# Kernel optimization log

Hardware: AMD Instinct MI355X
Metric: run time of the kernel (lower is better)

The kernel has to match this reference:

```python
import jax, jax.numpy as jnp
import numpy as np
import math

GROUPS = 32
EPS = 1e-5
N_HEADS = 8  # channels=512 / num_head_channels=64


def group_norm(x, w, b):
    # x: [B, C, T]; GroupNorm over (channels-in-group, T)
    B, C, T = x.shape
    xg = x.reshape(B, GROUPS, C // GROUPS * T)
    mu = xg.mean(axis=-1, keepdims=True)
    var = xg.var(axis=-1, keepdims=True)
    xn = ((xg - mu) * jax.lax.rsqrt(var + EPS)).reshape(B, C, T)
    return xn * w[None, :, None] + b[None, :, None]


def setup_inputs() -> dict:
    key = jax.random.key(0)
    ks = jax.random.split(key, 7)
    C = 512
    return {
        "x": jax.random.normal(ks[0], (8, C, 32, 32), dtype=jnp.float32),
        "norm_w": jax.random.normal(ks[1], (C,), dtype=jnp.float32),
        "norm_b": jax.random.normal(ks[2], (C,), dtype=jnp.float32),
        "qkv_w": jax.random.normal(ks[3], (3 * C, C), dtype=jnp.float32) * 0.02,
        "qkv_b": jax.random.normal(ks[4], (3 * C,), dtype=jnp.float32) * 0.02,
        "proj_w": jax.random.normal(ks[5], (C, C), dtype=jnp.float32) * 0.02,
        "proj_b": jax.random.normal(ks[6], (C,), dtype=jnp.float32) * 0.02,
    }


def reference(x, norm_w, norm_b, qkv_w, qkv_b, proj_w, proj_b):
    b, c, H, W = x.shape
    T = H * W
    xf = x.reshape(b, c, T)
    xn = group_norm(xf, norm_w, norm_b)
    # 1x1 conv1d == channel matmul: [3C, C] x [B, C, T] -> [B, 3C, T]
    qkv = jnp.einsum('oc,bct->bot', qkv_w, xn) + qkv_b[None, :, None]
    ch = c // N_HEADS
    qkv = qkv.reshape(b * N_HEADS, 3 * ch, T)
    q, k, v = qkv[:, :ch], qkv[:, ch:2 * ch], qkv[:, 2 * ch:]
    scale = 1.0 / math.sqrt(math.sqrt(ch))
    # [BH, T, T] score matrix (explicit, as in the original)
    weight = jnp.einsum('bct,bcs->bts', q * scale, k * scale)
    weight = jax.nn.softmax(weight.astype(jnp.float32), axis=-1).astype(qkv.dtype)
    a = jnp.einsum('bts,bcs->bct', weight, v).reshape(b, c, T)
    hout = jnp.einsum('oc,bct->bot', proj_w, a) + proj_b[None, :, None]
    return (xf + hout).reshape(b, c, H, W)
```

## Files before the change

### kernel.cpp

```cpp
#include <hip/hip_runtime.h>
#include <math.h>

typedef float f32x4_t __attribute__((ext_vector_type(4)));
typedef short bf16x8_t __attribute__((ext_vector_type(8)));

#define B_   8
#define C_   512
#define T_   1024
#define NH_  8
#define CH_  64
#define EPSF 1e-5f

#define MFMA16(a, b, c) __builtin_amdgcn_mfma_f32_16x16x32_bf16((a), (b), (c), 0, 0, 0)

__device__ __forceinline__ unsigned short f2bf(float f) {
  union { float f; unsigned u; } v; v.f = f;
  unsigned r = v.u + 0x7FFFu + ((v.u >> 16) & 1u);
  return (unsigned short)(r >> 16);
}

typedef const unsigned int u32_g __attribute__((address_space(1)));
typedef unsigned int u32_l __attribute__((address_space(3)));
__device__ __forceinline__ void gld16(const unsigned short* g, unsigned short* l) {
  __builtin_amdgcn_global_load_lds((u32_g*)g, (u32_l*)l, 16, 0, 0);
}
__device__ __forceinline__ void load_tile(const unsigned short* g,
                                          unsigned short* l, int tid) {
  int wb = (tid >> 6) * 512;
  gld16(g + tid * 8,        l + wb);
  gld16(g + 2048 + tid * 8, l + 2048 + wb);
}

__global__ __launch_bounds__(256) void prep_gn_kernel(
    const float* __restrict__ x, const float* __restrict__ w,
    const float* __restrict__ bvec, unsigned short* __restrict__ xnP,
    const float* __restrict__ qw_f, const float* __restrict__ pw_f,
    unsigned short* __restrict__ qwP, unsigned short* __restrict__ pwP)
{
  int tid = threadIdx.x;
  if (blockIdx.x >= 256) {
    int idx = (blockIdx.x - 256) * 256 + tid;
    const int N1 = 1536 * 512 / 4;
    const int N2 = 512 * 512 / 4;
    if (idx < N1) {
      float4 v = ((const float4*)qw_f)[idx];
      int o = idx >> 7, cq = (idx & 127) * 4;
      uint2 ov;
      ov.x = (unsigned)f2bf(v.x) | ((unsigned)f2bf(v.y) << 16);
      ov.y = (unsigned)f2bf(v.z) | ((unsigned)f2bf(v.w) << 16);
      *(uint2*)&qwP[((size_t)(cq >> 5) * 1536 + o) * 32 + (cq & 31)] = ov;
    } else if (idx < N1 + N2) {
      int j = idx - N1;
      float4 v = ((const float4*)pw_f)[j];
      int o = j >> 7, cq = (j & 127) * 4;
      uint2 ov;
      ov.x = (unsigned)f2bf(v.x) | ((unsigned)f2bf(v.y) << 16);
      ov.y = (unsigned)f2bf(v.z) | ((unsigned)f2bf(v.w) << 16);
      *(uint2*)&pwP[((size_t)(cq >> 5) * 512 + o) * 32 + (cq & 31)] = ov;
    }
    return;
  }

  int blk = blockIdx.x;
  int b = blk >> 5, g = blk & 31;
  const float* xp = x + ((size_t)(b * C_ + g * 16)) * T_;
  const int N = 16 * T_;

  float s = 0.f, s2 = 0.f;
  for (int i = tid * 4; i < N; i += 256 * 4) {
    float4 v = *(const float4*)(xp + i);
    s  += v.x + v.y + v.z + v.w;
    s2 += v.x * v.x + v.y * v.y + v.z * v.z + v.w * v.w;
  }
  for (int off = 32; off; off >>= 1) {
    s  += __shfl_down(s,  off, 64);
    s2 += __shfl_down(s2, off, 64);
  }
  __shared__ float rs_[4], r2_[4];
  __shared__ float mu_s, rsig_s;
  int wid = tid >> 6, lane = tid & 63;
  if (lane == 0) { rs_[wid] = s; r2_[wid] = s2; }
  __syncthreads();
  if (tid == 0) {
    float ts = rs_[0] + rs_[1] + rs_[2] + rs_[3];
    float t2 = r2_[0] + r2_[1] + r2_[2] + r2_[3];
    float mu = ts / (float)N;
    float var = t2 / (float)N - mu * mu;
    mu_s = mu;
    rsig_s = rsqrtf(var + EPSF);
  }
  __syncthreads();
  float mu = mu_s, rs = rsig_s;

  float wl[16], bl[16];
  for (int c = 0; c < 16; ++c) { wl[c] = w[g * 16 + c]; bl[c] = bvec[g * 16 + c]; }

  unsigned short* dbase = xnP + ((size_t)(b * 16 + (g >> 1)) * T_) * 32 + (g & 1) * 16;
  for (int t = tid; t < T_; t += 256) {
    unsigned short buf[16] __attribute__((aligned(16)));
    for (int c = 0; c < 16; ++c) {
      float val = xp[(size_t)c * T_ + t];
      buf[c] = f2bf((val - mu) * rs * wl[c] + bl[c]);
    }
    unsigned short* dst = dbase + (size_t)t * 32;
    *(uint4*)dst       = *(uint4*)buf;
    *(uint4*)(dst + 8) = *(uint4*)(buf + 8);
  }
}

__global__ __launch_bounds__(256) void gemm_qkv_kernel(
    const unsigned short* __restrict__ Wp, const unsigned short* __restrict__ xnP,
    const float* __restrict__ bias,
    unsigned short* __restrict__ q_t, unsigned short* __restrict__ k_t,
    unsigned short* __restrict__ v_c)
{
  int b = blockIdx.z;
  int m0 = blockIdx.y * 128, n0 = blockIdx.x * 128;
  int tid = threadIdx.x;
  int w = tid >> 6, lane = tid & 63, quad = lane >> 4, lr = lane & 15;
  int wm = w >> 1, wn = w & 1;

  __shared__ __align__(16) unsigned short As[2][128 * 32];
  __shared__ __align__(16) unsigned short Bs[2][128 * 32];

  f32x4_t acc[4][4];
  for (int i = 0; i < 4; ++i)
    for (int j = 0; j < 4; ++j) acc[i][j] = (f32x4_t){0.f, 0.f, 0.f, 0.f};

  const unsigned short* Abase = Wp + (size_t)m0 * 32;
  const unsigned short* Bbase = xnP + ((size_t)(b * 16) * T_ + n0) * 32;

  load_tile(Abase, As[0], tid);
  load_tile(Bbase, Bs[0], tid);

  for (int kp = 0; kp < 16; ++kp) {
    int cur = kp & 1;
    __syncthreads();
    if (kp < 15) {
      load_tile(Abase + (size_t)(kp + 1) * 1536 * 32, As[cur ^ 1], tid);
      load_tile(Bbase + (size_t)(kp + 1) * 1024 * 32, Bs[cur ^ 1], tid);
    }
    bf16x8_t af[4], bfv[4];
    for (int i = 0; i < 4; ++i)
      af[i]  = *(bf16x8_t*)&As[cur][(wm * 64 + i * 16 + lr) * 32 + quad * 8];
    for (int j = 0; j < 4; ++j)
      bfv[j] = *(bf16x8_t*)&Bs[cur][(wn * 64 + j * 16 + lr) * 32 + quad * 8];
    for (int i = 0; i < 4; ++i)
      for (int j = 0; j < 4; ++j)
        acc[i][j] = MFMA16(af[i], bfv[j], acc[i][j]);
  }

  for (int i = 0; i < 4; ++i) {
    int ob = m0 + wm * 64 + i * 16 + quad * 4;
    int h = ob / 192, r0 = ob % 192;
    for (int j = 0; j < 4; ++j) {
      int t = n0 + wn * 64 + j * 16 + lr;
      if (r0 < 128) {
        unsigned short pk[4] __attribute__((aligned(8)));
      #pragma unroll
        for (int r = 0; r < 4; ++r) pk[r] = f2bf(acc[i][j][r] + bias[ob + r]);
        unsigned short* base = (r0 < 64) ? q_t : k_t;
        int chn = (r0 < 64) ? r0 : r0 - 64;
        *(uint2*)&base[((size_t)(b * NH_ + h) * T_ + t) * CH_ + chn] = *(uint2*)pk;
      } else {
      #pragma unroll
        for (int r = 0; r < 4; ++r) {
          float vv = acc[i][j][r] + bias[ob + r];
          v_c[((size_t)(b * NH_ + h) * CH_ + (r0 - 128 + r)) * T_ + t] = f2bf(vv);
        }
      }
    }
  }
}

__global__ __launch_bounds__(256) void attn_kernel(
    const unsigned short* __restrict__ q_t, const unsigned short* __restrict__ k_t,
    const unsigned short* __restrict__ v_c, unsigned short* __restrict__ aP)
{
  int bh = blockIdx.x;
  int t0 = blockIdx.y * 64;
  int tid = threadIdx.x;
  int w = tid >> 6, lane = tid & 63, quad = lane >> 4, lr = lane & 15;

  __shared__ __align__(16) unsigned short q_s[64][72];
  __shared__ __align__(16) unsigned short k_s[64][72];
  __shared__ __align__(16) unsigned short v_s[64][72];
  __shared__ __align__(16) unsigned short p_s[64][72];

  int r0 = tid >> 3, c0 = (tid & 7) * 8;
  *(uint4*)&q_s[r0][c0] =
      *(const uint4*)&q_t[((size_t)bh * T_ + t0 + r0) * CH_ + c0];
  *(uint4*)&q_s[r0 + 32][c0] =
      *(const uint4*)&q_t[((size_t)bh * T_ + t0 + r0 + 32) * CH_ + c0];

  uint4 kr0 = *(const uint4*)&k_t[((size_t)bh * T_ + r0) * CH_ + c0];
  uint4 kr1 = *(const uint4*)&k_t[((size_t)bh * T_ + r0 + 32) * CH_ + c0];
  uint4 vr0 = *(const uint4*)&v_c[((size_t)bh * CH_ + r0) * T_ + c0];
  uint4 vr1 = *(const uint4*)&v_c[((size_t)bh * CH_ + r0 + 32) * T_ + c0];

  __syncthreads();
  bf16x8_t aq[2];
  aq[0] = *(bf16x8_t*)&q_s[w * 16 + lr][quad * 8];
  aq[1] = *(bf16x8_t*)&q_s[w * 16 + lr][32 + quad * 8];

  bf16x8_t ones8;
  {
    short ov = (lr == 0) ? (short)0x3F80 : (short)0;
    for (int e = 0; e < 8; ++e) ones8[e] = ov;
  }

  f32x4_t o_acc[4], o_l;
  for (int j = 0; j < 4; ++j) o_acc[j] = (f32x4_t){0.f, 0.f, 0.f, 0.f};
  o_l = (f32x4_t){0.f, 0.f, 0.f, 0.f};

  const float SCL = 0.18033688f;
  const float MSH = 11.541560f;

  for (int s0 = 0; s0 < T_; s0 += 64) {
    __syncthreads();
    *(uint4*)&k_s[r0][c0]      = kr0;
    *(uint4*)&k_s[r0 + 32][c0] = kr1;
    *(uint4*)&v_s[r0][c0]      = vr0;
    *(uint4*)&v_s[r0 + 32][c0] = vr1;
    if (s0 + 64 < T_) {
      kr0 = *(const uint4*)&k_t[((size_t)bh * T_ + s0 + 64 + r0) * CH_ + c0];
      kr1 = *(const uint4*)&k_t[((size_t)bh * T_ + s0 + 96 + r0) * CH_ + c0];
      vr0 = *(const uint4*)&v_c[((size_t)bh * CH_ + r0) * T_ + s0 + 64 + c0];
      vr1 = *(const uint4*)&v_c[((size_t)bh * CH_ + r0 + 32) * T_ + s0 + 64 + c0];
    }
    __syncthreads();

    f32x4_t sc[4];
    for (int j = 0; j < 4; ++j) {
      f32x4_t a2 = (f32x4_t){0.f, 0.f, 0.f, 0.f};
      for (int kk = 0; kk < 2; ++kk) {
        bf16x8_t bk = *(bf16x8_t*)&k_s[j * 16 + lr][kk * 32 + quad * 8];
        a2 = MFMA16(aq[kk], bk, a2);
      }
      sc[j] = a2;
    }

    for (int j = 0; j < 4; ++j)
      for (int r = 0; r < 4; ++r) {
        float p = __builtin_amdgcn_exp2f(sc[j][r] * SCL - MSH);
        union { float f; unsigned u; } cv; cv.f = p;
        p_s[w * 16 + quad * 4 + r][j * 16 + lr] = (unsigned short)(cv.u >> 16);
      }
    bf16x8_t ap[2];
    ap[0] = *(bf16x8_t*)&p_s[w * 16 + lr][quad * 8];
    ap[1] = *(bf16x8_t*)&p_s[w * 16 + lr][32 + quad * 8];

    o_l = MFMA16(ap[0], ones8, o_l);
    o_l = MFMA16(ap[1], ones8, o_l);
    for (int j = 0; j < 4; ++j)
      for (int kk = 0; kk < 2; ++kk) {
        bf16x8_t bv = *(bf16x8_t*)&v_s[j * 16 + lr][kk * 32 + quad * 8];
        o_acc[j] = MFMA16(ap[kk], bv, o_acc[j]);
      }
  }

  float lv[4];
  for (int r = 0; r < 4; ++r) lv[r] = __shfl(o_l[r], lane & 48, 64);
  for (int r = 0; r < 4; ++r) {
    float inv = 1.f / lv[r];
    for (int j = 0; j < 4; ++j)
      q_s[w * 16 + quad * 4 + r][j * 16 + lr] = f2bf(o_acc[j][r] * inv);
  }
  __syncthreads();
  {
    int b = bh >> 3, h = bh & 7;
    size_t pb = (size_t)(b * 16 + h * 2 + (c0 >= 32 ? 1 : 0)) * T_;
    int cc = c0 & 31;
    *(uint4*)&aP[(pb + t0 + r0) * 32 + cc]      = *(uint4*)&q_s[r0][c0];
    *(uint4*)&aP[(pb + t0 + r0 + 32) * 32 + cc] = *(uint4*)&q_s[r0 + 32][c0];
  }
}

__global__ __launch_bounds__(256) void gemm_proj_kernel(
    const unsigned short* __restrict__ Wp, const unsigned short* __restrict__ aP,
    const float* __restrict__ bias, const float* __restrict__ xres,
    float* __restrict__ out)
{
  int b = blockIdx.z;
  int m0 = blockIdx.y * 128, n0 = blockIdx.x * 128;
  int tid = threadIdx.x;
  int w = tid >> 6, lane = tid & 63, quad = lane >> 4, lr = lane & 15;
  int wm = w >> 1, wn = w & 1;

  __shared__ __align__(16) unsigned short As[2][128 * 32];
  __shared__ __align__(16) unsigned short Bs[2][128 * 32];

  f32x4_t acc[4][4];
  for (int i = 0; i < 4; ++i)
    for (int j = 0; j < 4; ++j) acc[i][j] = (f32x4_t){0.f, 0.f, 0.f, 0.f};

  const unsigned short* Abase = Wp + (size_t)m0 * 32;
  const unsigned short* Bbase = aP + ((size_t)(b * 16) * T_ + n0) * 32;

  load_tile(Abase, As[0], tid);
  load_tile(Bbase, Bs[0], tid);

  for (int kp = 0; kp < 16; ++kp) {
    int cur = kp & 1;
    __syncthreads();
    if (kp < 15) {
      load_tile(Abase + (size_t)(kp + 1) * 512 * 32, As[cur ^ 1], tid);
      load_tile(Bbase + (size_t)(kp + 1) * 1024 * 32, Bs[cur ^ 1], tid);
    }
    bf16x8_t af[4], bfv[4];
    for (int i = 0; i < 4; ++i)
      af[i]  = *(bf16x8_t*)&As[cur][(wm * 64 + i * 16 + lr) * 32 + quad * 8];
    for (int j = 0; j < 4; ++j)
      bfv[j] = *(bf16x8_t*)&Bs[cur][(wn * 64 + j * 16 + lr) * 32 + quad * 8];
    for (int i = 0; i < 4; ++i)
      for (int j = 0; j < 4; ++j)
        acc[i][j] = MFMA16(af[i], bfv[j], acc[i][j]);
  }

  for (int i = 0; i < 4; ++i) {
    int ob = m0 + wm * 64 + i * 16 + quad * 4;
    for (int j = 0; j < 4; ++j) {
      int t = n0 + wn * 64 + j * 16 + lr;
    #pragma unroll
      for (int r = 0; r < 4; ++r) {
        size_t idx = ((size_t)(b * C_ + ob + r)) * T_ + t;
        out[idx] = acc[i][j][r] + bias[ob + r] + xres[idx];
      }
    }
  }
}

extern "C" void kernel_launch(void* const* d_in, const int* in_sizes, int n_in,
                              void* d_out, int out_size, void* d_ws, size_t ws_size,
                              hipStream_t stream)
{
  const float* x      = (const float*)d_in[0];
  const float* norm_w = (const float*)d_in[1];
  const float* norm_b = (const float*)d_in[2];
  const float* qkv_w  = (const float*)d_in[3];
  const float* qkv_b  = (const float*)d_in[4];
  const float* proj_w = (const float*)d_in[5];
  const float* proj_b = (const float*)d_in[6];
  float* out = (float*)d_out;

  char* ws = (char*)d_ws;
  unsigned short* qwP = (unsigned short*)ws;
  unsigned short* pwP = (unsigned short*)(ws + 1572864);
  unsigned short* xnP = (unsigned short*)(ws + 2097152);
  unsigned short* q_t = (unsigned short*)(ws + 10485760);
  unsigned short* k_t = (unsigned short*)(ws + 18874368);
  unsigned short* v_c = (unsigned short*)(ws + 27262976);
  unsigned short* aP  = (unsigned short*)(ws + 35651584);

  prep_gn_kernel<<<dim3(256 + 1024), dim3(256), 0, stream>>>(
      x, norm_w, norm_b, xnP, qkv_w, proj_w, qwP, pwP);

  gemm_qkv_kernel<<<dim3(T_ / 128, 1536 / 128, B_), dim3(256), 0, stream>>>(
      qwP, xnP, qkv_b, q_t, k_t, v_c);

  attn_kernel<<<dim3(B_ * NH_, T_ / 64), dim3(256), 0, stream>>>(q_t, k_t, v_c, aP);

  gemm_proj_kernel<<<dim3(T_ / 128, C_ / 128, B_), dim3(256), 0, stream>>>(
      pwP, aP, proj_b, x, out);
}
```

Baseline: 167.2 us.

## Register-cache groupnorm input and stage QKV epilogue through LDS for coalesced stores

The groupnorm kernel now loads its 16x1024 slice into registers once and reuses it for both the statistics pass and the normalize/pack pass, so x is read from global memory once instead of twice. The QKV GEMM epilogue writes q/k tiles into a padded LDS staging buffer (reusing the A/B tile memory) and then stores them with 16-byte coalesced writes, replacing scattered 8-byte stores. This adds an extra barrier and more register pressure in the norm kernel, and the v path still uses strided 2-byte stores.

```diff
diff --git a/kernel.cpp b/kernel.cpp
--- a/kernel.cpp
+++ b/kernel.cpp
@@ -64,11 +64,16 @@
   int blk = blockIdx.x;
   int b = blk >> 5, g = blk & 31;
   const float* xp = x + ((size_t)(b * C_ + g * 16)) * T_;
-  const int N = 16 * T_;
+
+  float4 xr[16];
+#pragma unroll
+  for (int k = 0; k < 16; ++k)
+    xr[k] = *(const float4*)(xp + (size_t)k * T_ + tid * 4);
 
   float s = 0.f, s2 = 0.f;
-  for (int i = tid * 4; i < N; i += 256 * 4) {
-    float4 v = *(const float4*)(xp + i);
+#pragma unroll
+  for (int k = 0; k < 16; ++k) {
+    float4 v = xr[k];
     s  += v.x + v.y + v.z + v.w;
     s2 += v.x * v.x + v.y * v.y + v.z * v.z + v.w * v.w;
   }
@@ -84,8 +89,9 @@
   if (tid == 0) {
     float ts = rs_[0] + rs_[1] + rs_[2] + rs_[3];
     float t2 = r2_[0] + r2_[1] + r2_[2] + r2_[3];
-    float mu = ts / (float)N;
-    float var = t2 / (float)N - mu * mu;
+    const float N = 16.f * 1024.f;
+    float mu = ts / N;
+    float var = t2 / N - mu * mu;
     mu_s = mu;
     rsig_s = rsqrtf(var + EPSF);
   }
@@ -93,14 +99,18 @@
   float mu = mu_s, rs = rsig_s;
 
   float wl[16], bl[16];
+#pragma unroll
   for (int c = 0; c < 16; ++c) { wl[c] = w[g * 16 + c]; bl[c] = bvec[g * 16 + c]; }
 
   unsigned short* dbase = xnP + ((size_t)(b * 16 + (g >> 1)) * T_) * 32 + (g & 1) * 16;
-  for (int t = tid; t < T_; t += 256) {
+#pragma unroll
+  for (int j = 0; j < 4; ++j) {
+    int t = tid * 4 + j;
     unsigned short buf[16] __attribute__((aligned(16)));
-    for (int c = 0; c < 16; ++c) {
-      float val = xp[(size_t)c * T_ + t];
-      buf[c] = f2bf((val - mu) * rs * wl[c] + bl[c]);
+#pragma unroll
+    for (int k = 0; k < 16; ++k) {
+      float val = ((const float*)&xr[k])[j];
+      buf[k] = f2bf((val - mu) * rs * wl[k] + bl[k]);
     }
     unsigned short* dst = dbase + (size_t)t * 32;
     *(uint4*)dst       = *(uint4*)buf;
@@ -120,8 +130,11 @@
   int w = tid >> 6, lane = tid & 63, quad = lane >> 4, lr = lane & 15;
   int wm = w >> 1, wn = w & 1;
 
-  __shared__ __align__(16) unsigned short As[2][128 * 32];
-  __shared__ __align__(16) unsigned short Bs[2][128 * 32];
+  __shared__ __align__(16) unsigned short smem[17408];
+  unsigned short* As0 = smem;
+  unsigned short* As1 = smem + 4096;
+  unsigned short* Bs0 = smem + 8192;
+  unsigned short* Bs1 = smem + 12288;
 
   f32x4_t acc[4][4];
   for (int i = 0; i < 4; ++i)
@@ -130,45 +143,70 @@
   const unsigned short* Abase = Wp + (size_t)m0 * 32;
   const unsigned short* Bbase = xnP + ((size_t)(b * 16) * T_ + n0) * 32;
 
-  load_tile(Abase, As[0], tid);
-  load_tile(Bbase, Bs[0], tid);
+  load_tile(Abase, As0, tid);
+  load_tile(Bbase, Bs0, tid);
 
   for (int kp = 0; kp < 16; ++kp) {
-    int cur = kp & 1;
+    unsigned short* Ac = (kp & 1) ? As1 : As0;
+    unsigned short* Bc = (kp & 1) ? Bs1 : Bs0;
     __syncthreads();
     if (kp < 15) {
-      load_tile(Abase + (size_t)(kp + 1) * 1536 * 32, As[cur ^ 1], tid);
-      load_tile(Bbase + (size_t)(kp + 1) * 1024 * 32, Bs[cur ^ 1], tid);
+      load_tile(Abase + (size_t)(kp + 1) * 1536 * 32, (kp & 1) ? As0 : As1, tid);
+      load_tile(Bbase + (size_t)(kp + 1) * 1024 * 32, (kp & 1) ? Bs0 : Bs1, tid);
     }
     bf16x8_t af[4], bfv[4];
     for (int i = 0; i < 4; ++i)
-      af[i]  = *(bf16x8_t*)&As[cur][(wm * 64 + i * 16 + lr) * 32 + quad * 8];
+      af[i]  = *(bf16x8_t*)&Ac[(wm * 64 + i * 16 + lr) * 32 + quad * 8];
     for (int j = 0; j < 4; ++j)
-      bfv[j] = *(bf16x8_t*)&Bs[cur][(wn * 64 + j * 16 + lr) * 32 + quad * 8];
+      bfv[j] = *(bf16x8_t*)&Bc[(wn * 64 + j * 16 + lr) * 32 + quad * 8];
     for (int i = 0; i < 4; ++i)
       for (int j = 0; j < 4; ++j)
         acc[i][j] = MFMA16(af[i], bfv[j], acc[i][j]);
   }
 
-  for (int i = 0; i < 4; ++i) {
-    int ob = m0 + wm * 64 + i * 16 + quad * 4;
-    int h = ob / 192, r0 = ob % 192;
-    for (int j = 0; j < 4; ++j) {
-      int t = n0 + wn * 64 + j * 16 + lr;
-      if (r0 < 128) {
-        unsigned short pk[4] __attribute__((aligned(8)));
-      #pragma unroll
-        for (int r = 0; r < 4; ++r) pk[r] = f2bf(acc[i][j][r] + bias[ob + r]);
-        unsigned short* base = (r0 < 64) ? q_t : k_t;
-        int chn = (r0 < 64) ? r0 : r0 - 64;
-        *(uint2*)&base[((size_t)(b * NH_ + h) * T_ + t) * CH_ + chn] = *(uint2*)pk;
-      } else {
+  __syncthreads();
+
+  int secbase = m0 + wm * 64;
+  int h = secbase / 192, r0 = secbase % 192;
+
+  if (r0 == 128) {
+    for (int i = 0; i < 4; ++i) {
+      int ob = secbase + i * 16 + quad * 4;
+      for (int j = 0; j < 4; ++j) {
+        int t = n0 + wn * 64 + j * 16 + lr;
       #pragma unroll
         for (int r = 0; r < 4; ++r) {
           float vv = acc[i][j][r] + bias[ob + r];
-          v_c[((size_t)(b * NH_ + h) * CH_ + (r0 - 128 + r)) * T_ + t] = f2bf(vv);
+          v_c[((size_t)(b * NH_ + h) * CH_ + (ob - secbase + r)) * T_ + t] = f2bf(vv);
         }
       }
+    }
+  } else {
+    unsigned short* st = smem + wm * (128 * 68);
+    for (int i = 0; i < 4; ++i) {
+      int ol = i * 16 + quad * 4;
+      for (int j = 0; j < 4; ++j) {
+        int tl = wn * 64 + j * 16 + lr;
+        unsigned short pk[4] __attribute__((aligned(8)));
+      #pragma unroll
+        for (int r = 0; r < 4; ++r) pk[r] = f2bf(acc[i][j][r] + bias[secbase + ol + r]);
+        *(uint2*)&st[tl * 68 + ol] = *(uint2*)pk;
+      }
+    }
+  }
+  __syncthreads();
+
+  for (int sec = 0; sec < 2; ++sec) {
+    int sb = m0 + sec * 64;
+    int hh = sb / 192, rr = sb % 192;
+    if (rr == 128) continue;
+    unsigned short* dst = ((rr == 0) ? q_t : k_t) +
+                          ((size_t)(b * NH_ + hh) * T_ + n0) * CH_;
+    const unsigned short* st = smem + sec * (128 * 68);
+    for (int u = 0; u < 4; ++u) {
+      int idx = u * 256 + tid;
+      int tl = idx >> 3, c8 = (idx & 7) * 8;
+      *(uint4*)&dst[(size_t)tl * CH_ + c8] = *(const uint4*)&st[tl * 68 + c8];
     }
   }
 }
```

After: 164.5 us. Within noise of the previous version (-1.7%).
